# Kernel tuning notes

Hardware: AMD Instinct MI355X
Metric: run time of the kernel (lower is better)

Reference implementation:

```python
import jax, jax.numpy as jnp
import numpy as np

NUM_HEADS = 6
TAU = 1.0


def _split_heads(y, h):
    b, n, c = y.shape
    return y.reshape(b, n, h, c // h).transpose(0, 2, 1, 3)  # b h n d


def setup_inputs() -> dict:
    key = jax.random.key(0)
    B, M, C = 8, 1026, 384
    names = ["Wq1", "Wq2", "Wk1", "Wk2", "Wv1", "Wv2", "Wo"]
    ks = jax.random.split(key, len(names) + 3)
    inp = {"x": jax.random.normal(ks[0], (B, M, C), jnp.float32)}
    for i, nm in enumerate(names):
        inp[nm] = jax.random.normal(ks[i + 1], (C, C), jnp.float32) * 0.02
        inp["b" + nm[1:]] = jnp.zeros((C,), jnp.float32)
    inp["weights"] = jax.random.normal(ks[-2], (4,), jnp.float32)
    u = jax.random.uniform(ks[-1], (4,), jnp.float32, 1e-6, 1.0 - 1e-6)
    inp["gumbel_noise"] = -jnp.log(-jnp.log(u))  # fixed gumbel sample for determinism
    return inp


def reference(x, Wq1, bq1, Wq2, bq2, Wk1, bk1, Wk2, bk2,
              Wv1, bv1, Wv2, bv2, Wo, bo, weights, gumbel_noise):
    B, M, C = x.shape
    N1 = (M - 2) // 2 + 1  # N + 1, quadrant size
    h = NUM_HEADS
    d = C // h
    scale = d ** -0.5
    x1, x2 = x[:, :N1], x[:, N1:]
    q = jnp.concatenate([_split_heads(x1 @ Wq1 + bq1, h),
                         _split_heads(x2 @ Wq2 + bq2, h)], axis=2)  # b h M d
    k = jnp.concatenate([_split_heads(x1 @ Wk1 + bk1, h),
                         _split_heads(x2 @ Wk2 + bk2, h)], axis=2)
    v1 = _split_heads(x1 @ Wv1 + bv1, h)  # b h N1 d
    v2 = _split_heads(x2 @ Wv2 + bv2, h)
    attn = jnp.einsum('bhqd,bhkd->bhqk', q, k) * scale  # b h M M
    b1 = jax.nn.softmax(attn[:, :, :N1, :N1], axis=-1)
    b2 = jax.nn.softmax(attn[:, :, :N1, N1:], axis=-1)
    b3 = jax.nn.softmax(attn[:, :, N1:, :N1], axis=-1)
    b4 = jax.nn.softmax(attn[:, :, N1:, N1:], axis=-1)
    # hard gumbel-softmax gate (straight-through)
    y_soft = jax.nn.softmax((weights + gumbel_noise) / TAU)
    y_hard = jax.nn.one_hot(jnp.argmax(y_soft), 4, dtype=y_soft.dtype)
    w = y_hard + y_soft - jax.lax.stop_gradient(y_soft)
    A = w[0] * b1 + w[1] * b2 + w[2] * b3 + w[3] * b4  # b h N1 N1
    out1 = jnp.einsum('bhqk,bhkd->bhqd', A, v1)
    out2 = jnp.einsum('bhqk,bhkd->bhqd', A, v2)
    out = jnp.concatenate([out1, out2], axis=2)  # b h M d
    out = out.transpose(0, 2, 1, 3).reshape(B, M, C)
    return out @ Wo + bo
```

## Files before the change

kernel.cpp:

```cpp
#include <hip/hip_runtime.h>

typedef unsigned short u16;
typedef short v8s __attribute__((ext_vector_type(8)));
typedef float v4f __attribute__((ext_vector_type(4)));

namespace {
constexpr int kC = 384;
constexpr int kN1 = 513;
constexpr int kH = 6;
constexpr int kBH = 48;
constexpr int kRows = 4104;
constexpr int kRows2 = 8208;
constexpr int kPld = 576;
}

__device__ __forceinline__ u16 f2b(float f) {
  unsigned int u = __float_as_uint(f);
  u += 0x7fffu + ((u >> 16) & 1u);
  return (u16)(u >> 16);
}

__device__ __forceinline__ int gumbel_argmax(const float* __restrict__ w,
                                             const float* __restrict__ g) {
  float v0 = w[0] + g[0], v1 = w[1] + g[1], v2 = w[2] + g[2], v3 = w[3] + g[3];
  int j = 0;
  float m = v0;
  if (v1 > m) { m = v1; j = 1; }
  if (v2 > m) { m = v2; j = 2; }
  if (v3 > m) { m = v3; j = 3; }
  return j;
}

__global__ __launch_bounds__(256) void prep(
    const float* __restrict__ x, const float* __restrict__ Wq1,
    const float* __restrict__ Wq2, const float* __restrict__ Wk1,
    const float* __restrict__ Wk2, const float* __restrict__ Wv1,
    const float* __restrict__ Wv2, const float* __restrict__ Wo,
    const float* __restrict__ wts, const float* __restrict__ gum,
    u16* __restrict__ xb, u16* __restrict__ Wqt, u16* __restrict__ Wkt,
    u16* __restrict__ Wv1t, u16* __restrict__ Wv2t, u16* __restrict__ Wot) {
  __shared__ float tb[32][33];
  const int bx = blockIdx.x;
  if (bx < 720) {
    const int z = bx / 144, rem = bx - z * 144;
    const int c0 = (rem % 12) * 32, r0 = (rem / 12) * 32;
    const int j = gumbel_argmax(wts, gum);
    const float* src;
    u16* dst;
    switch (z) {
      case 0: src = (j < 2) ? Wq1 : Wq2; dst = Wqt; break;
      case 1: src = (j == 0 || j == 2) ? Wk1 : Wk2; dst = Wkt; break;
      case 2: src = Wv1; dst = Wv1t; break;
      case 3: src = Wv2; dst = Wv2t; break;
      default: src = Wo; dst = Wot; break;
    }
    const int tx = threadIdx.x & 31, ty = threadIdx.x >> 5;
    for (int p = 0; p < 4; ++p)
      tb[ty + p * 8][tx] = src[(size_t)(r0 + ty + p * 8) * kC + c0 + tx];
    __syncthreads();
    for (int p = 0; p < 4; ++p)
      dst[(size_t)(c0 + ty + p * 8) * kC + r0 + tx] = f2b(tb[tx][ty + p * 8]);
  } else {
    const size_t i = ((size_t)(bx - 720) * 256 + threadIdx.x) * 8;
    if (i >= (size_t)kRows2 * kC) return;
    const float4 a = *(const float4*)(x + i);
    const float4 b = *(const float4*)(x + i + 4);
    v8s o = {(short)f2b(a.x), (short)f2b(a.y), (short)f2b(a.z), (short)f2b(a.w),
             (short)f2b(b.x), (short)f2b(b.y), (short)f2b(b.z), (short)f2b(b.w)};
    *(v8s*)(xb + i) = o;
  }
}

__global__ __launch_bounds__(256) void qkv_mfma(
    const u16* __restrict__ xb, const u16* __restrict__ Wqt,
    const u16* __restrict__ Wkt, const u16* __restrict__ Wv1t,
    const u16* __restrict__ Wv2t, const float* __restrict__ bq1,
    const float* __restrict__ bq2, const float* __restrict__ bk1,
    const float* __restrict__ bk2, const float* __restrict__ bv1,
    const float* __restrict__ bv2, const float* __restrict__ wts,
    const float* __restrict__ gum, u16* __restrict__ Qb, u16* __restrict__ Kb,
    u16* __restrict__ Vt1, u16* __restrict__ Vt2) {
  __shared__ __align__(16) u16 As[128][72];
  __shared__ __align__(16) u16 Bs[128][72];
  const int op = blockIdx.z;
  const int j = gumbel_argmax(wts, gum);
  const bool vmode = (op >= 2);
  const float* bias;
  int xoff;
  const u16* Wt;
  if (op == 0) {
    bias = (j < 2) ? bq1 : bq2; xoff = (j < 2) ? 0 : kN1; Wt = Wqt;
  } else if (op == 1) {
    const bool u1 = (j == 0 || j == 2);
    bias = u1 ? bk1 : bk2; xoff = u1 ? 0 : kN1; Wt = Wkt;
  } else if (op == 2) {
    bias = bv1; xoff = 0; Wt = Wv1t;
  } else {
    bias = bv2; xoff = kN1; Wt = Wv2t;
  }
  const int mb = vmode ? blockIdx.y : blockIdx.x;
  const int nb = vmode ? blockIdx.x : blockIdx.y;
  const int m0 = mb * 128, n0 = nb * 128;
  const int tid = threadIdx.x;
  const int lane = tid & 63, l16 = lane & 15, quad = lane >> 4;
  const int wv = tid >> 6, wr = wv >> 1, wc = wv & 1;
  const int sr = tid >> 2, sc = (tid & 3) * 16;

  v4f acc[4][4];
  const v4f z4 = {0.f, 0.f, 0.f, 0.f};
  for (int i = 0; i < 4; ++i)
    for (int n = 0; n < 4; ++n) acc[i][n] = z4;

  for (int k0 = 0; k0 < kC; k0 += 64) {
    for (int p = 0; p < 2; ++p) {
      const int r = p * 64 + sr;
      v8s v0 = {0, 0, 0, 0, 0, 0, 0, 0}, v1 = v0;
      if (!vmode) {
        const int t = m0 + r;
        if (t < kRows) {
          const int bb = t / kN1, mm = t - bb * kN1;
          const u16* s = xb + ((size_t)(bb * 1026 + xoff + mm)) * kC + k0 + sc;
          v0 = *(const v8s*)s;
          v1 = *(const v8s*)(s + 8);
        }
      } else {
        const u16* s = Wt + (size_t)(m0 + r) * kC + k0 + sc;
        v0 = *(const v8s*)s;
        v1 = *(const v8s*)(s + 8);
      }
      *(v8s*)&As[r][sc] = v0;
      *(v8s*)&As[r][sc + 8] = v1;
    }
    for (int p = 0; p < 2; ++p) {
      const int r = p * 64 + sr;
      v8s v0 = {0, 0, 0, 0, 0, 0, 0, 0}, v1 = v0;
      if (!vmode) {
        const u16* s = Wt + (size_t)(n0 + r) * kC + k0 + sc;
        v0 = *(const v8s*)s;
        v1 = *(const v8s*)(s + 8);
      } else {
        const int t = n0 + r;
        if (t < kRows) {
          const int bb = t / kN1, mm = t - bb * kN1;
          const u16* s = xb + ((size_t)(bb * 1026 + xoff + mm)) * kC + k0 + sc;
          v0 = *(const v8s*)s;
          v1 = *(const v8s*)(s + 8);
        }
      }
      *(v8s*)&Bs[r][sc] = v0;
      *(v8s*)&Bs[r][sc + 8] = v1;
    }
    __syncthreads();
    for (int ks = 0; ks < 2; ++ks) {
      v8s af[4], bfr[4];
      for (int i = 0; i < 4; ++i)
        af[i] = *(const v8s*)&As[wr * 64 + i * 16 + l16][ks * 32 + quad * 8];
      for (int n = 0; n < 4; ++n)
        bfr[n] = *(const v8s*)&Bs[wc * 64 + n * 16 + l16][ks * 32 + quad * 8];
      for (int i = 0; i < 4; ++i)
        for (int n = 0; n < 4; ++n)
          acc[i][n] = __builtin_amdgcn_mfma_f32_16x16x32_bf16(af[i], bfr[n],
                                                              acc[i][n], 0, 0, 0);
    }
    __syncthreads();
  }

  if (!vmode) {
    u16* outp = (op == 0) ? Qb : Kb;
    const float osc = (op == 0) ? 0.125f : 1.0f;
    float bv4[4];
    for (int nt = 0; nt < 4; ++nt) bv4[nt] = bias[n0 + wc * 64 + nt * 16 + l16];
    for (int i = 0; i < 4; ++i) {
      const int rowb = m0 + wr * 64 + i * 16 + quad * 4;
      for (int r = 0; r < 4; ++r) {
        const int row = rowb + r;
        if (row >= kRows) continue;
        for (int nt = 0; nt < 4; ++nt) {
          const int col = n0 + wc * 64 + nt * 16 + l16;
          outp[(size_t)row * kC + col] = f2b((acc[i][nt][r] + bv4[nt]) * osc);
        }
      }
    }
  } else {
    u16* Vt = (op == 2) ? Vt1 : Vt2;
    for (int nt = 0; nt < 4; ++nt) {
      const int t = n0 + wc * 64 + nt * 16 + l16;
      if (t >= kRows) continue;
      const int bb = t / kN1, mm = t - bb * kN1;
      for (int i = 0; i < 4; ++i) {
        const int colb = m0 + wr * 64 + i * 16 + quad * 4;
        for (int r = 0; r < 4; ++r) {
          const int col = colb + r;
          const int hh = col >> 6, d = col & 63;
          Vt[((size_t)(bb * kH + hh) * 64 + d) * kPld + mm] =
              f2b(acc[i][nt][r] + bias[col]);
        }
      }
    }
  }
}

__global__ __launch_bounds__(256) void attn_fused(const u16* __restrict__ Qb,
                                                  const u16* __restrict__ Kb,
                                                  const u16* __restrict__ Vt1,
                                                  const u16* __restrict__ Vt2,
                                                  u16* __restrict__ PRE) {
  __shared__ __align__(16) u16 Qs[64][72];
  __shared__ __align__(16) u16 Ks[64][72];
  __shared__ __align__(16) u16 Vs[128][72];
  __shared__ __align__(16) u16 Ps[4][16][72];
  const int bh = blockIdx.y;
  const int b = bh / kH, hh = bh - b * kH;
  const int q0 = blockIdx.x * 64;
  const int tid = threadIdx.x;
  const int w = tid >> 6, lane = tid & 63, l16 = lane & 15, quad = lane >> 4;
  const v8s z8 = {0, 0, 0, 0, 0, 0, 0, 0};
  {
    const int r = tid >> 2, sc = (tid & 3) * 16;
    const int q = q0 + r;
    v8s v0 = z8, v1 = z8;
    if (q < kN1) {
      const u16* s = Qb + ((size_t)(b * kN1 + q)) * kC + hh * 64 + sc;
      v0 = *(const v8s*)s;
      v1 = *(const v8s*)(s + 8);
    }
    *(v8s*)&Qs[r][sc] = v0;
    *(v8s*)&Qs[r][sc + 8] = v1;
  }
  float lsum[4] = {0.f, 0.f, 0.f, 0.f};
  v4f Oacc[8];
  const v4f z4 = {0.f, 0.f, 0.f, 0.f};
  for (int n = 0; n < 8; ++n) Oacc[n] = z4;

  for (int kt = 0; kt < 9; ++kt) {
    const int k0 = kt * 64;
    __syncthreads();
    {
      const int r = tid >> 2, sc = (tid & 3) * 16;
      const int ki = k0 + r;
      v8s v0 = z8, v1 = z8;
      if (ki < kN1) {
        const u16* s = Kb + ((size_t)(b * kN1 + ki)) * kC + hh * 64 + sc;
        v0 = *(const v8s*)s;
        v1 = *(const v8s*)(s + 8);
      }
      *(v8s*)&Ks[r][sc] = v0;
      *(v8s*)&Ks[r][sc + 8] = v1;
    }
    {
      const int d = tid >> 1, c0 = (tid & 1) * 32;
      const u16* src = (d < 64) ? (Vt1 + ((size_t)bh * 64 + d) * kPld)
                                : (Vt2 + ((size_t)bh * 64 + (d - 64)) * kPld);
      for (int p = 0; p < 4; ++p)
        *(v8s*)&Vs[d][c0 + p * 8] = *(const v8s*)(src + k0 + c0 + p * 8);
    }
    __syncthreads();
    v4f sacc[4];
    for (int nt = 0; nt < 4; ++nt) sacc[nt] = z4;
    for (int kc = 0; kc < 2; ++kc) {
      const v8s aq = *(const v8s*)&Qs[w * 16 + l16][kc * 32 + quad * 8];
      for (int nt = 0; nt < 4; ++nt) {
        const v8s bk = *(const v8s*)&Ks[nt * 16 + l16][kc * 32 + quad * 8];
        sacc[nt] = __builtin_amdgcn_mfma_f32_16x16x32_bf16(aq, bk, sacc[nt], 0, 0, 0);
      }
    }
    for (int r = 0; r < 4; ++r) {
      float ps = 0.f;
      for (int nt = 0; nt < 4; ++nt) {
        const int col = k0 + nt * 16 + l16;
        const float p = (col < kN1) ? __expf(sacc[nt][r]) : 0.f;
        ps += p;
        Ps[w][quad * 4 + r][nt * 16 + l16] = f2b(p);
      }
      lsum[r] += ps;
    }
    for (int kc = 0; kc < 2; ++kc) {
      const v8s ap = *(const v8s*)&Ps[w][l16][kc * 32 + quad * 8];
      for (int n = 0; n < 8; ++n) {
        const v8s bv = *(const v8s*)&Vs[n * 16 + l16][kc * 32 + quad * 8];
        Oacc[n] = __builtin_amdgcn_mfma_f32_16x16x32_bf16(ap, bv, Oacc[n], 0, 0, 0);
      }
    }
  }
  float rinv[4];
  for (int r = 0; r < 4; ++r) {
    float s = lsum[r];
    for (int o = 1; o <= 8; o <<= 1) s += __shfl_xor(s, o);
    rinv[r] = 1.f / s;
  }
  for (int n = 0; n < 8; ++n) {
    const int col = hh * 64 + (n & 3) * 16 + l16;
    const int rbase = b * 1026 + ((n < 4) ? 0 : kN1);
    for (int r = 0; r < 4; ++r) {
      const int q = q0 + w * 16 + quad * 4 + r;
      if (q >= kN1) continue;
      PRE[(size_t)(rbase + q) * kC + col] = f2b(Oacc[n][r] * rinv[r]);
    }
  }
}

__global__ __launch_bounds__(256) void out_mfma(const u16* __restrict__ PRE,
                                                const u16* __restrict__ Wot,
                                                const float* __restrict__ bo,
                                                float* __restrict__ OUT) {
  __shared__ __align__(16) u16 As[128][72];
  __shared__ __align__(16) u16 Bs[128][72];
  const int m0 = blockIdx.x * 128, n0 = blockIdx.y * 128;
  const int tid = threadIdx.x;
  const int lane = tid & 63, l16 = lane & 15, quad = lane >> 4;
  const int wv = tid >> 6, wr = wv >> 1, wc = wv & 1;
  const int sr = tid >> 2, sc = (tid & 3) * 16;
  v4f acc[4][4];
  const v4f z4 = {0.f, 0.f, 0.f, 0.f};
  for (int i = 0; i < 4; ++i)
    for (int n = 0; n < 4; ++n) acc[i][n] = z4;
  for (int k0 = 0; k0 < kC; k0 += 64) {
    for (int p = 0; p < 2; ++p) {
      const int r = p * 64 + sr;
      v8s v0 = {0, 0, 0, 0, 0, 0, 0, 0}, v1 = v0;
      const int row = m0 + r;
      if (row < kRows2) {
        const u16* s = PRE + (size_t)row * kC + k0 + sc;
        v0 = *(const v8s*)s;
        v1 = *(const v8s*)(s + 8);
      }
      *(v8s*)&As[r][sc] = v0;
      *(v8s*)&As[r][sc + 8] = v1;
      const u16* s2 = Wot + (size_t)(n0 + r) * kC + k0 + sc;
      *(v8s*)&Bs[r][sc] = *(const v8s*)s2;
      *(v8s*)&Bs[r][sc + 8] = *(const v8s*)(s2 + 8);
    }
    __syncthreads();
    for (int ks = 0; ks < 2; ++ks) {
      v8s af[4], bfr[4];
      for (int i = 0; i < 4; ++i)
        af[i] = *(const v8s*)&As[wr * 64 + i * 16 + l16][ks * 32 + quad * 8];
      for (int n = 0; n < 4; ++n)
        bfr[n] = *(const v8s*)&Bs[wc * 64 + n * 16 + l16][ks * 32 + quad * 8];
      for (int i = 0; i < 4; ++i)
        for (int n = 0; n < 4; ++n)
          acc[i][n] = __builtin_amdgcn_mfma_f32_16x16x32_bf16(af[i], bfr[n],
                                                              acc[i][n], 0, 0, 0);
    }
    __syncthreads();
  }
  float bv4[4];
  for (int nt = 0; nt < 4; ++nt) bv4[nt] = bo[n0 + wc * 64 + nt * 16 + l16];
  for (int i = 0; i < 4; ++i) {
    const int rowb = m0 + wr * 64 + i * 16 + quad * 4;
    for (int r = 0; r < 4; ++r) {
      const int row = rowb + r;
      if (row >= kRows2) continue;
      for (int nt = 0; nt < 4; ++nt) {
        const int col = n0 + wc * 64 + nt * 16 + l16;
        OUT[(size_t)row * kC + col] = acc[i][nt][r] + bv4[nt];
      }
    }
  }
}

extern "C" void kernel_launch(void* const* d_in, const int* in_sizes, int n_in,
                              void* d_out, int out_size, void* d_ws,
                              size_t ws_size, hipStream_t stream) {
  const float* x = (const float*)d_in[0];
  const float* Wq1 = (const float*)d_in[1];
  const float* bq1 = (const float*)d_in[2];
  const float* Wq2 = (const float*)d_in[3];
  const float* bq2 = (const float*)d_in[4];
  const float* Wk1 = (const float*)d_in[5];
  const float* bk1 = (const float*)d_in[6];
  const float* Wk2 = (const float*)d_in[7];
  const float* bk2 = (const float*)d_in[8];
  const float* Wv1 = (const float*)d_in[9];
  const float* bv1 = (const float*)d_in[10];
  const float* Wv2 = (const float*)d_in[11];
  const float* bv2 = (const float*)d_in[12];
  const float* Wo = (const float*)d_in[13];
  const float* bo = (const float*)d_in[14];
  const float* wts = (const float*)d_in[15];
  const float* gum = (const float*)d_in[16];

  u16* xb = (u16*)d_ws;
  u16* Wqt = xb + (size_t)kRows2 * kC;
  u16* Wkt = Wqt + 147456;
  u16* Wv1t = Wkt + 147456;
  u16* Wv2t = Wv1t + 147456;
  u16* Wot = Wv2t + 147456;
  u16* Qb = Wot + 147456;
  u16* Kb = Qb + (size_t)kRows * kC;
  u16* Vt1 = Kb + (size_t)kRows * kC;
  u16* Vt2 = Vt1 + (size_t)kBH * 64 * kPld;
  u16* PRE = Vt2 + (size_t)kBH * 64 * kPld;

  prep<<<dim3(2260), 256, 0, stream>>>(x, Wq1, Wq2, Wk1, Wk2, Wv1, Wv2, Wo, wts,
                                       gum, xb, Wqt, Wkt, Wv1t, Wv2t, Wot);
  qkv_mfma<<<dim3(33, 3, 4), 256, 0, stream>>>(
      xb, Wqt, Wkt, Wv1t, Wv2t, bq1, bq2, bk1, bk2, bv1, bv2, wts, gum, Qb, Kb,
      Vt1, Vt2);
  attn_fused<<<dim3(9, kBH), 256, 0, stream>>>(Qb, Kb, Vt1, Vt2, PRE);
  out_mfma<<<dim3(65, 3), 256, 0, stream>>>(PRE, Wot, bo, (float*)d_out);
}
```

Before: 153.0 us.

## Fuse x bf16 conversion into QKV GEMM and prefetch K/V tiles in attention

Result: no change. 151.0 us (-1.3%).

```diff
diff --git a/kernel.cpp b/kernel.cpp
--- a/kernel.cpp
+++ b/kernel.cpp
@@ -31,48 +31,38 @@
   return j;
 }
 
-__global__ __launch_bounds__(256) void prep(
-    const float* __restrict__ x, const float* __restrict__ Wq1,
-    const float* __restrict__ Wq2, const float* __restrict__ Wk1,
-    const float* __restrict__ Wk2, const float* __restrict__ Wv1,
-    const float* __restrict__ Wv2, const float* __restrict__ Wo,
-    const float* __restrict__ wts, const float* __restrict__ gum,
-    u16* __restrict__ xb, u16* __restrict__ Wqt, u16* __restrict__ Wkt,
-    u16* __restrict__ Wv1t, u16* __restrict__ Wv2t, u16* __restrict__ Wot) {
+__global__ __launch_bounds__(256) void prep_w(
+    const float* __restrict__ Wq1, const float* __restrict__ Wq2,
+    const float* __restrict__ Wk1, const float* __restrict__ Wk2,
+    const float* __restrict__ Wv1, const float* __restrict__ Wv2,
+    const float* __restrict__ Wo, const float* __restrict__ wts,
+    const float* __restrict__ gum, u16* __restrict__ Wqt,
+    u16* __restrict__ Wkt, u16* __restrict__ Wv1t, u16* __restrict__ Wv2t,
+    u16* __restrict__ Wot) {
   __shared__ float tb[32][33];
   const int bx = blockIdx.x;
-  if (bx < 720) {
-    const int z = bx / 144, rem = bx - z * 144;
-    const int c0 = (rem % 12) * 32, r0 = (rem / 12) * 32;
-    const int j = gumbel_argmax(wts, gum);
-    const float* src;
-    u16* dst;
-    switch (z) {
-      case 0: src = (j < 2) ? Wq1 : Wq2; dst = Wqt; break;
-      case 1: src = (j == 0 || j == 2) ? Wk1 : Wk2; dst = Wkt; break;
-      case 2: src = Wv1; dst = Wv1t; break;
-      case 3: src = Wv2; dst = Wv2t; break;
-      default: src = Wo; dst = Wot; break;
-    }
-    const int tx = threadIdx.x & 31, ty = threadIdx.x >> 5;
-    for (int p = 0; p < 4; ++p)
-      tb[ty + p * 8][tx] = src[(size_t)(r0 + ty + p * 8) * kC + c0 + tx];
-    __syncthreads();
-    for (int p = 0; p < 4; ++p)
-      dst[(size_t)(c0 + ty + p * 8) * kC + r0 + tx] = f2b(tb[tx][ty + p * 8]);
-  } else {
-    const size_t i = ((size_t)(bx - 720) * 256 + threadIdx.x) * 8;
-    if (i >= (size_t)kRows2 * kC) return;
-    const float4 a = *(const float4*)(x + i);
-    const float4 b = *(const float4*)(x + i + 4);
-    v8s o = {(short)f2b(a.x), (short)f2b(a.y), (short)f2b(a.z), (short)f2b(a.w),
-             (short)f2b(b.x), (short)f2b(b.y), (short)f2b(b.z), (short)f2b(b.w)};
-    *(v8s*)(xb + i) = o;
-  }
+  const int z = bx / 144, rem = bx - z * 144;
+  const int c0 = (rem % 12) * 32, r0 = (rem / 12) * 32;
+  const int j = gumbel_argmax(wts, gum);
+  const float* src;
+  u16* dst;
+  switch (z) {
+    case 0: src = (j < 2) ? Wq1 : Wq2; dst = Wqt; break;
+    case 1: src = (j == 0 || j == 2) ? Wk1 : Wk2; dst = Wkt; break;
+    case 2: src = Wv1; dst = Wv1t; break;
+    case 3: src = Wv2; dst = Wv2t; break;
+    default: src = Wo; dst = Wot; break;
+  }
+  const int tx = threadIdx.x & 31, ty = threadIdx.x >> 5;
+  for (int p = 0; p < 4; ++p)
+    tb[ty + p * 8][tx] = src[(size_t)(r0 + ty + p * 8) * kC + c0 + tx];
+  __syncthreads();
+  for (int p = 0; p < 4; ++p)
+    dst[(size_t)(c0 + ty + p * 8) * kC + r0 + tx] = f2b(tb[tx][ty + p * 8]);
 }
 
 __global__ __launch_bounds__(256) void qkv_mfma(
-    const u16* __restrict__ xb, const u16* __restrict__ Wqt,
+    const float* __restrict__ x, const u16* __restrict__ Wqt,
     const u16* __restrict__ Wkt, const u16* __restrict__ Wv1t,
     const u16* __restrict__ Wv2t, const float* __restrict__ bq1,
     const float* __restrict__ bq2, const float* __restrict__ bk1,
@@ -119,9 +109,17 @@
         const int t = m0 + r;
         if (t < kRows) {
           const int bb = t / kN1, mm = t - bb * kN1;
-          const u16* s = xb + ((size_t)(bb * 1026 + xoff + mm)) * kC + k0 + sc;
-          v0 = *(const v8s*)s;
-          v1 = *(const v8s*)(s + 8);
+          const float* s = x + ((size_t)(bb * 1026 + xoff + mm)) * kC + k0 + sc;
+          const float4 f0 = *(const float4*)s;
+          const float4 f1 = *(const float4*)(s + 4);
+          const float4 f2 = *(const float4*)(s + 8);
+          const float4 f3 = *(const float4*)(s + 12);
+          v0 = (v8s){(short)f2b(f0.x), (short)f2b(f0.y), (short)f2b(f0.z),
+                     (short)f2b(f0.w), (short)f2b(f1.x), (short)f2b(f1.y),
+                     (short)f2b(f1.z), (short)f2b(f1.w)};
+          v1 = (v8s){(short)f2b(f2.x), (short)f2b(f2.y), (short)f2b(f2.z),
+                     (short)f2b(f2.w), (short)f2b(f3.x), (short)f2b(f3.y),
+                     (short)f2b(f3.z), (short)f2b(f3.w)};
         }
       } else {
         const u16* s = Wt + (size_t)(m0 + r) * kC + k0 + sc;
@@ -142,9 +140,17 @@
         const int t = n0 + r;
         if (t < kRows) {
           const int bb = t / kN1, mm = t - bb * kN1;
-          const u16* s = xb + ((size_t)(bb * 1026 + xoff + mm)) * kC + k0 + sc;
-          v0 = *(const v8s*)s;
-          v1 = *(const v8s*)(s + 8);
+          const float* s = x + ((size_t)(bb * 1026 + xoff + mm)) * kC + k0 + sc;
+          const float4 f0 = *(const float4*)s;
+          const float4 f1 = *(const float4*)(s + 4);
+          const float4 f2 = *(const float4*)(s + 8);
+          const float4 f3 = *(const float4*)(s + 12);
+          v0 = (v8s){(short)f2b(f0.x), (short)f2b(f0.y), (short)f2b(f0.z),
+                     (short)f2b(f0.w), (short)f2b(f1.x), (short)f2b(f1.y),
+                     (short)f2b(f1.z), (short)f2b(f1.w)};
+          v1 = (v8s){(short)f2b(f2.x), (short)f2b(f2.y), (short)f2b(f2.z),
+                     (short)f2b(f2.w), (short)f2b(f3.x), (short)f2b(f3.y),
+                     (short)f2b(f3.z), (short)f2b(f3.w)};
         }
       }
       *(v8s*)&Bs[r][sc] = v0;
@@ -205,7 +211,6 @@
                                                   const u16* __restrict__ Vt1,
                                                   const u16* __restrict__ Vt2,
                                                   u16* __restrict__ PRE) {
-  __shared__ __align__(16) u16 Qs[64][72];
   __shared__ __align__(16) u16 Ks[64][72];
   __shared__ __align__(16) u16 Vs[128][72];
   __shared__ __align__(16) u16 Ps[4][16][72];
@@ -214,18 +219,29 @@
   const int q0 = blockIdx.x * 64;
   const int tid = threadIdx.x;
   const int w = tid >> 6, lane = tid & 63, l16 = lane & 15, quad = lane >> 4;
-  const v8s z8 = {0, 0, 0, 0, 0, 0, 0, 0};
+  v8s aq0, aq1;
   {
-    const int r = tid >> 2, sc = (tid & 3) * 16;
-    const int q = q0 + r;
-    v8s v0 = z8, v1 = z8;
-    if (q < kN1) {
-      const u16* s = Qb + ((size_t)(b * kN1 + q)) * kC + hh * 64 + sc;
-      v0 = *(const v8s*)s;
-      v1 = *(const v8s*)(s + 8);
-    }
-    *(v8s*)&Qs[r][sc] = v0;
-    *(v8s*)&Qs[r][sc + 8] = v1;
+    int qr = q0 + w * 16 + l16;
+    if (qr > 512) qr = 512;
+    const u16* qs = Qb + ((size_t)(b * kN1 + qr)) * kC + hh * 64 + quad * 8;
+    aq0 = *(const v8s*)qs;
+    aq1 = *(const v8s*)(qs + 32);
+  }
+  const int ksr = tid >> 2, ksc = (tid & 3) * 16;
+  const int vd = tid >> 1, vc = (tid & 1) * 32;
+  const u16* kbase = Kb + (size_t)b * kN1 * kC + hh * 64 + ksc;
+  const u16* vbase = ((vd < 64) ? (Vt1 + ((size_t)bh * 64 + vd) * kPld)
+                                : (Vt2 + ((size_t)bh * 64 + (vd - 64)) * kPld)) +
+                     vc;
+  v8s kr0, kr1, vr0, vr1, vr2, vr3;
+  {
+    const u16* s = kbase + (size_t)ksr * kC;
+    kr0 = *(const v8s*)s;
+    kr1 = *(const v8s*)(s + 8);
+    vr0 = *(const v8s*)(vbase);
+    vr1 = *(const v8s*)(vbase + 8);
+    vr2 = *(const v8s*)(vbase + 16);
+    vr3 = *(const v8s*)(vbase + 24);
   }
   float lsum[4] = {0.f, 0.f, 0.f, 0.f};
   v4f Oacc[8];
@@ -235,34 +251,32 @@
   for (int kt = 0; kt < 9; ++kt) {
     const int k0 = kt * 64;
     __syncthreads();
-    {
-      const int r = tid >> 2, sc = (tid & 3) * 16;
-      const int ki = k0 + r;
-      v8s v0 = z8, v1 = z8;
-      if (ki < kN1) {
-        const u16* s = Kb + ((size_t)(b * kN1 + ki)) * kC + hh * 64 + sc;
-        v0 = *(const v8s*)s;
-        v1 = *(const v8s*)(s + 8);
-      }
-      *(v8s*)&Ks[r][sc] = v0;
-      *(v8s*)&Ks[r][sc + 8] = v1;
-    }
-    {
-      const int d = tid >> 1, c0 = (tid & 1) * 32;
-      const u16* src = (d < 64) ? (Vt1 + ((size_t)bh * 64 + d) * kPld)
-                                : (Vt2 + ((size_t)bh * 64 + (d - 64)) * kPld);
-      for (int p = 0; p < 4; ++p)
-        *(v8s*)&Vs[d][c0 + p * 8] = *(const v8s*)(src + k0 + c0 + p * 8);
-    }
-    __syncthreads();
+    *(v8s*)&Ks[ksr][ksc] = kr0;
+    *(v8s*)&Ks[ksr][ksc + 8] = kr1;
+    *(v8s*)&Vs[vd][vc] = vr0;
+    *(v8s*)&Vs[vd][vc + 8] = vr1;
+    *(v8s*)&Vs[vd][vc + 16] = vr2;
+    *(v8s*)&Vs[vd][vc + 24] = vr3;
+    __syncthreads();
+    if (kt < 8) {
+      int ki = k0 + 64 + ksr;
+      if (ki > 512) ki = 512;
+      const u16* s = kbase + (size_t)ki * kC;
+      kr0 = *(const v8s*)s;
+      kr1 = *(const v8s*)(s + 8);
+      const u16* t = vbase + k0 + 64;
+      vr0 = *(const v8s*)t;
+      vr1 = *(const v8s*)(t + 8);
+      vr2 = *(const v8s*)(t + 16);
+      vr3 = *(const v8s*)(t + 24);
+    }
     v4f sacc[4];
     for (int nt = 0; nt < 4; ++nt) sacc[nt] = z4;
-    for (int kc = 0; kc < 2; ++kc) {
-      const v8s aq = *(const v8s*)&Qs[w * 16 + l16][kc * 32 + quad * 8];
-      for (int nt = 0; nt < 4; ++nt) {
-        const v8s bk = *(const v8s*)&Ks[nt * 16 + l16][kc * 32 + quad * 8];
-        sacc[nt] = __builtin_amdgcn_mfma_f32_16x16x32_bf16(aq, bk, sacc[nt], 0, 0, 0);
-      }
+    for (int nt = 0; nt < 4; ++nt) {
+      const v8s bk0 = *(const v8s*)&Ks[nt * 16 + l16][quad * 8];
+      sacc[nt] = __builtin_amdgcn_mfma_f32_16x16x32_bf16(aq0, bk0, sacc[nt], 0, 0, 0);
+      const v8s bk1 = *(const v8s*)&Ks[nt * 16 + l16][32 + quad * 8];
+      sacc[nt] = __builtin_amdgcn_mfma_f32_16x16x32_bf16(aq1, bk1, sacc[nt], 0, 0, 0);
     }
     for (int r = 0; r < 4; ++r) {
       float ps = 0.f;
@@ -380,8 +394,7 @@
   const float* wts = (const float*)d_in[15];
   const float* gum = (const float*)d_in[16];
 
-  u16* xb = (u16*)d_ws;
-  u16* Wqt = xb + (size_t)kRows2 * kC;
+  u16* Wqt = (u16*)d_ws;
   u16* Wkt = Wqt + 147456;
   u16* Wv1t = Wkt + 147456;
   u16* Wv2t = Wv1t + 147456;
@@ -392,10 +405,10 @@
   u16* Vt2 = Vt1 + (size_t)kBH * 64 * kPld;
   u16* PRE = Vt2 + (size_t)kBH * 64 * kPld;
 
-  prep<<<dim3(2260), 256, 0, stream>>>(x, Wq1, Wq2, Wk1, Wk2, Wv1, Wv2, Wo, wts,
-                                       gum, xb, Wqt, Wkt, Wv1t, Wv2t, Wot);
+  prep_w<<<dim3(720), 256, 0, stream>>>(Wq1, Wq2, Wk1, Wk2, Wv1, Wv2, Wo, wts,
+                                        gum, Wqt, Wkt, Wv1t, Wv2t, Wot);
   qkv_mfma<<<dim3(33, 3, 4), 256, 0, stream>>>(
-      xb, Wqt, Wkt, Wv1t, Wv2t, bq1, bq2, bk1, bk2, bv1, bv2, wts, gum, Qb, Kb,
+      x, Wqt, Wkt, Wv1t, Wv2t, bq1, bq2, bk1, bk2, bv1, bv2, wts, gum, Qb, Kb,
       Vt1, Vt2);
   attn_fused<<<dim3(9, kBH), 256, 0, stream>>>(Qb, Kb, Vt1, Vt2, PRE);
   out_mfma<<<dim3(65, 3), 256, 0, stream>>>(PRE, Wot, bo, (float*)d_out);
```
